# Kernel optimization log

Hardware: AMD Instinct MI355X
Metric: run time of the kernel (lower is better)

## Reference

```python
import jax, jax.numpy as jnp
import numpy as np

D_MODEL = 1024
N_HEADS = 16

def setup_inputs() -> dict:
    key = jax.random.key(0)
    ks = jax.random.split(key, 11)
    B, L, S, D = 2, 2048, 2048, D_MODEL
    s = 1.0 / np.sqrt(D)
    return {
        "Q": jax.random.normal(ks[0], (B, L, D), jnp.float32),
        "K": jax.random.normal(ks[1], (B, S, D), jnp.float32),
        "V": jax.random.normal(ks[2], (B, S, D), jnp.float32),
        "Wq": jax.random.normal(ks[3], (D, D), jnp.float32) * s,
        "bq": jnp.zeros((D,), jnp.float32),
        "Wk": jax.random.normal(ks[4], (D, D), jnp.float32) * s,
        "bk": jnp.zeros((D,), jnp.float32),
        "Wv": jax.random.normal(ks[5], (D, D), jnp.float32) * s,
        "bv": jnp.zeros((D,), jnp.float32),
        "We": jax.random.normal(ks[6], (D, D), jnp.float32) * s,
        "be": jnp.zeros((D,), jnp.float32),
    }

def reference(Q, K, V, Wq, bq, Wk, bk, Wv, bv, We, be):
    B, L, D = Q.shape
    S = K.shape[1]
    H = N_HEADS
    E = D // H
    # projections, split heads
    q = (Q @ Wq + bq).reshape(B, L, H, E)
    k = (K @ Wk + bk).reshape(B, S, H, E)
    v = (V @ Wv + bv).reshape(B, S, H, E)
    scale = 1.0 / np.sqrt(E)
    scores = jnp.einsum('blhe,bshe->bhls', q, k)  # [B,H,L,S]
    A = jax.nn.softmax(scale * scores, axis=-1)   # dropout is identity in eval
    out = jnp.einsum('bhls,bshd->blhd', A, v).reshape(B, L, H * E)
    return out @ We + be
```

## Files before the change

kernel.cpp:

```cpp
#include <hip/hip_runtime.h>
#include <hip/hip_bf16.h>
#include <stdint.h>

typedef __bf16 bf16_t;
typedef bf16_t bf16x8 __attribute__((ext_vector_type(8)));
typedef float  f32x4  __attribute__((ext_vector_type(4)));
typedef float  f32x16 __attribute__((ext_vector_type(16)));

#define GLOAD16(gp, lp) __builtin_amdgcn_global_load_lds( \
    (const __attribute__((address_space(1))) void*)(gp),  \
    (__attribute__((address_space(3))) void*)(lp), 16, 0, 0)

#define EXP2F(x) __builtin_amdgcn_exp2f(x)

__device__ inline uint32_t pack2(float lo, float hi) {
    union { bf16_t h[2]; uint32_t u; } x;
    x.h[0] = (bf16_t)lo; x.h[1] = (bf16_t)hi;
    return x.u;
}

__global__ __launch_bounds__(256) void wtrans_kernel(
    const float* __restrict__ Wq, const float* __restrict__ Wk,
    const float* __restrict__ Wv, const float* __restrict__ We,
    bf16_t* __restrict__ WqT, bf16_t* __restrict__ WkT,
    bf16_t* __restrict__ WvT, bf16_t* __restrict__ WeT)
{
    __shared__ bf16_t T[64][65];
    const float* W = (blockIdx.z == 0) ? Wq : (blockIdx.z == 1) ? Wk
                   : (blockIdx.z == 2) ? Wv : We;
    bf16_t* O = (blockIdx.z == 0) ? WqT : (blockIdx.z == 1) ? WkT
              : (blockIdx.z == 2) ? WvT : WeT;
    const int k0 = blockIdx.y * 64, n0 = blockIdx.x * 64;
    const int t = threadIdx.x;
    for (int i = 0; i < 16; ++i) {
        int flat = t + i * 256;
        int r = flat >> 6, c = flat & 63;
        T[r][c] = (bf16_t)W[(size_t)(k0 + r) * 1024 + n0 + c];
    }
    __syncthreads();
    for (int i = 0; i < 16; ++i) {
        int flat = t + i * 256;
        int n = flat >> 6, kk = flat & 63;
        O[(size_t)(n0 + n) * 1024 + k0 + kk] = T[kk][n];
    }
}

__global__ __launch_bounds__(256)
void cvt_kernel(const float* __restrict__ X0, const float* __restrict__ X1,
                const float* __restrict__ X2,
                bf16_t* __restrict__ Y0, bf16_t* __restrict__ Y1,
                bf16_t* __restrict__ Y2)
{
    const float* X = (blockIdx.y == 0) ? X0 : (blockIdx.y == 1) ? X1 : X2;
    bf16_t*      Y = (blockIdx.y == 0) ? Y0 : (blockIdx.y == 1) ? Y1 : Y2;
    size_t i0 = ((size_t)blockIdx.x * 256 + threadIdx.x) * 8;
    float4 v0 = *(const float4*)(X + i0);
    float4 v1 = *(const float4*)(X + i0 + 4);
    bf16x8 pv;
    pv[0] = (bf16_t)v0.x; pv[1] = (bf16_t)v0.y;
    pv[2] = (bf16_t)v0.z; pv[3] = (bf16_t)v0.w;
    pv[4] = (bf16_t)v1.x; pv[5] = (bf16_t)v1.y;
    pv[6] = (bf16_t)v1.z; pv[7] = (bf16_t)v1.w;
    *(bf16x8*)(Y + i0) = pv;
}

template<bool BATCHED>
__global__ __launch_bounds__(256)
void gemm3_kernel(const bf16_t* __restrict__ A0, const bf16_t* __restrict__ A1,
                  const bf16_t* __restrict__ A2,
                  const bf16_t* __restrict__ B0, const bf16_t* __restrict__ B1,
                  const bf16_t* __restrict__ B2,
                  const float* __restrict__ b0, const float* __restrict__ b1,
                  const float* __restrict__ b2,
                  void* __restrict__ C0, void* __restrict__ C1,
                  void* __restrict__ C2)
{
    constexpr int M = 4096, K = 1024, N = 1024;
    __shared__ bf16_t As[128 * 64];
    __shared__ bf16_t Bs[128 * 64];

    const int msel = BATCHED ? blockIdx.y : 0;
    const bf16_t* Ab   = (msel == 0) ? A0 : (msel == 1) ? A1 : A2;
    const bf16_t* Bt   = (msel == 0) ? B0 : (msel == 1) ? B1 : B2;
    const float*  bias = (msel == 0) ? b0 : (msel == 1) ? b1 : b2;
    void*         Cv   = (msel == 0) ? C0 : (msel == 1) ? C1 : C2;
    const int omode = BATCHED ? ((msel == 2) ? 2 : 0) : 1;

    const int xcd = blockIdx.x & 7, idx = blockIdx.x >> 3;
    const int bm = (xcd << 2) | (idx >> 3), bn = idx & 7;
    const int row0 = bm * 128, col0 = bn * 128;
    const int t = threadIdx.x, w = t >> 6, l = t & 63;
    const int wr = w >> 1, wc = w & 1;

    f32x4 acc[4][4];
    #pragma unroll
    for (int i = 0; i < 4; ++i)
        #pragma unroll
        for (int j = 0; j < 4; ++j)
            #pragma unroll
            for (int c = 0; c < 4; ++c) acc[i][j][c] = 0.f;

    for (int k0 = 0; k0 < K; k0 += 64) {
        #pragma unroll
        for (int i = 0; i < 4; ++i) {
            int chunk = (w * 4 + i) * 64 + l;
            int r = chunk >> 3, c = chunk & 7;
            int soff = (c ^ (r & 7)) * 8;
            GLOAD16(Ab + (size_t)(row0 + r) * K + k0 + soff, &As[(w * 4 + i) * 512]);
            GLOAD16(Bt + (size_t)(col0 + r) * K + k0 + soff, &Bs[(w * 4 + i) * 512]);
        }
        __syncthreads();

        #pragma unroll
        for (int eks = 0; eks < 2; ++eks) {
            bf16x8 af[4], bfv[4];
            #pragma unroll
            for (int mi = 0; mi < 4; ++mi) {
                int row = wr * 64 + mi * 16 + (l & 15);
                int sl = (eks * 4 + (l >> 4)) ^ (row & 7);
                af[mi] = *(const bf16x8*)&As[row * 64 + sl * 8];
            }
            #pragma unroll
            for (int ni = 0; ni < 4; ++ni) {
                int row = wc * 64 + ni * 16 + (l & 15);
                int sl = (eks * 4 + (l >> 4)) ^ (row & 7);
                bfv[ni] = *(const bf16x8*)&Bs[row * 64 + sl * 8];
            }
            __builtin_amdgcn_s_setprio(1);
            #pragma unroll
            for (int mi = 0; mi < 4; ++mi)
                #pragma unroll
                for (int ni = 0; ni < 4; ++ni)
                    acc[mi][ni] = __builtin_amdgcn_mfma_f32_16x16x32_bf16(
                        af[mi], bfv[ni], acc[mi][ni], 0, 0, 0);
            __builtin_amdgcn_s_setprio(0);
        }
        __syncthreads();
    }

    #pragma unroll
    for (int mi = 0; mi < 4; ++mi)
        #pragma unroll
        for (int ni = 0; ni < 4; ++ni) {
            int col = col0 + wc * 64 + ni * 16 + (l & 15);
            float bv = bias[col];
            int rowb = row0 + wr * 64 + mi * 16 + (l >> 4) * 4;
            if (omode == 2) {
                union { bf16_t h[4]; uint64_t q; } pk;
                #pragma unroll
                for (int j = 0; j < 4; ++j)
                    pk.h[j] = (bf16_t)(acc[mi][ni][j] + bv);
                *(uint64_t*)((bf16_t*)Cv + (size_t)col * M + rowb) = pk.q;
            } else if (omode == 1) {
                #pragma unroll
                for (int j = 0; j < 4; ++j)
                    ((float*)Cv)[(size_t)(rowb + j) * N + col] = acc[mi][ni][j] + bv;
            } else {
                #pragma unroll
                for (int j = 0; j < 4; ++j)
                    ((bf16_t*)Cv)[(size_t)(rowb + j) * N + col] = (bf16_t)(acc[mi][ni][j] + bv);
            }
        }
}

__global__ __launch_bounds__(256)
void attn7_kernel(const bf16_t* __restrict__ qp, const bf16_t* __restrict__ kp,
                  const bf16_t* __restrict__ vT, bf16_t* __restrict__ o)
{
    __shared__ bf16_t Ks[2][4096];
    __shared__ bf16_t Vs[2][4096];
    const int bid = blockIdx.x;
    const int xcd = bid & 7, j = bid >> 3;
    const int bh = (xcd << 2) | (j & 3);
    const int qb = j >> 2;
    const int b = bh >> 4, h = bh & 15;
    const int t = threadIdx.x, w = t >> 6, l = t & 63;
    const int ql = l & 31, hh = l >> 5;
    const float M0 = 8.0f * 1.44269504f;

    const bf16_t* kbase = kp + ((size_t)b * 2048) * 1024 + h * 64;
    const bf16_t* vbase = vT + ((size_t)h * 64) * 4096 + (size_t)b * 2048;
    const int q0 = qb * 128 + w * 32;

    bf16x8 qf[4];
    {
        const bf16_t* qrow = qp + ((size_t)b * 2048 + q0 + ql) * 1024 + h * 64;
        const float qs = 0.125f * 1.44269504f;
        #pragma unroll
        for (int eks = 0; eks < 4; ++eks) {
            bf16x8 v = *(const bf16x8*)(qrow + eks * 16 + hh * 8);
            #pragma unroll
            for (int jj = 0; jj < 8; ++jj) v[jj] = (bf16_t)((float)v[jj] * qs);
            qf[eks] = v;
        }
    }

    f32x16 acc0, acc1;
    #pragma unroll
    for (int r = 0; r < 16; ++r) { acc0[r] = 0.f; acc1[r] = 0.f; }
    float lsum = 0.f;

    const int ci0 = (w * 2) * 64 + l, ci1 = (w * 2 + 1) * 64 + l;
    const int gr0 = ci0 >> 3, gc0 = ci0 & 7, so0 = ((gc0 ^ (gr0 & 7)) * 8);
    const int gr1 = ci1 >> 3, gc1 = ci1 & 7, so1 = ((gc1 ^ (gr1 & 7)) * 8);

    GLOAD16(kbase + (size_t)gr0 * 1024 + so0, &Ks[0][(w * 2) * 512]);
    GLOAD16(kbase + (size_t)gr1 * 1024 + so1, &Ks[0][(w * 2 + 1) * 512]);
    GLOAD16(vbase + (size_t)gr0 * 4096 + so0, &Vs[0][(w * 2) * 512]);
    GLOAD16(vbase + (size_t)gr1 * 4096 + so1, &Vs[0][(w * 2 + 1) * 512]);
    __syncthreads();

    int cur = 0;
    for (int tile = 0; tile < 32; ++tile) {
        if (tile + 1 < 32) {
            const int s1 = (tile + 1) * 64;
            GLOAD16(kbase + (size_t)(s1 + gr0) * 1024 + so0, &Ks[cur ^ 1][(w * 2) * 512]);
            GLOAD16(kbase + (size_t)(s1 + gr1) * 1024 + so1, &Ks[cur ^ 1][(w * 2 + 1) * 512]);
            GLOAD16(vbase + (size_t)gr0 * 4096 + s1 + so0, &Vs[cur ^ 1][(w * 2) * 512]);
            GLOAD16(vbase + (size_t)gr1 * 4096 + s1 + so1, &Vs[cur ^ 1][(w * 2 + 1) * 512]);
        }

        f32x16 sA, sB;
        #pragma unroll
        for (int r = 0; r < 16; ++r) { sA[r] = -M0; sB[r] = -M0; }
        __builtin_amdgcn_s_setprio(1);
        #pragma unroll
        for (int eks = 0; eks < 4; ++eks) {
            bf16x8 k0 = *(const bf16x8*)&Ks[cur][ql * 64 + (((2 * eks + hh) ^ (ql & 7)) * 8)];
            bf16x8 k1 = *(const bf16x8*)&Ks[cur][(32 + ql) * 64 + (((2 * eks + hh) ^ (ql & 7)) * 8)];
            sA = __builtin_amdgcn_mfma_f32_32x32x16_bf16(k0, qf[eks], sA, 0, 0, 0);
            sB = __builtin_amdgcn_mfma_f32_32x32x16_bf16(k1, qf[eks], sB, 0, 0, 0);
        }
        __builtin_amdgcn_s_setprio(0);

        uint32_t wA[8], wB[8];
        float rs = 0.f;
        #pragma unroll
        for (int i = 0; i < 8; ++i) {
            float p0 = EXP2F(sA[2 * i]);
            float p1 = EXP2F(sA[2 * i + 1]);
            rs += p0 + p1;  wA[i] = pack2(p0, p1);
            float p2 = EXP2F(sB[2 * i]);
            float p3 = EXP2F(sB[2 * i + 1]);
            rs += p2 + p3;  wB[i] = pack2(p2, p3);
        }
        rs += __shfl_xor(rs, 32);
        lsum += rs;

        #pragma unroll
        for (int ks = 0; ks < 4; ++ks) {
            const int base = (ks & 1) * 4;
            uint32_t a0 = (ks < 2) ? wA[base]     : wB[base];
            uint32_t a1 = (ks < 2) ? wA[base + 1] : wB[base + 1];
            uint32_t a2 = (ks < 2) ? wA[base + 2] : wB[base + 2];
            uint32_t a3 = (ks < 2) ? wA[base + 3] : wB[base + 3];
            asm volatile("v_permlane32_swap_b32 %0, %1" : "+v"(a0), "+v"(a2));
            asm volatile("v_permlane32_swap_b32 %0, %1" : "+v"(a1), "+v"(a3));
            union { uint32_t u[4]; bf16x8 v; } pb;
            pb.u[0] = a0; pb.u[1] = a1; pb.u[2] = a2; pb.u[3] = a3;
            bf16x8 v0 = *(const bf16x8*)&Vs[cur][ql * 64 + (((2 * ks + hh) ^ (ql & 7)) * 8)];
            bf16x8 v1 = *(const bf16x8*)&Vs[cur][(32 + ql) * 64 + (((2 * ks + hh) ^ (ql & 7)) * 8)];
            __builtin_amdgcn_s_setprio(1);
            acc0 = __builtin_amdgcn_mfma_f32_32x32x16_bf16(v0, pb.v, acc0, 0, 0, 0);
            acc1 = __builtin_amdgcn_mfma_f32_32x32x16_bf16(v1, pb.v, acc1, 0, 0, 0);
            __builtin_amdgcn_s_setprio(0);
        }

        __syncthreads();
        cur ^= 1;
    }

    bf16_t* sc = &Ks[0][0];
    const float inv = 1.0f / lsum;
    #pragma unroll
    for (int r = 0; r < 16; ++r) {
        int e = (r & 3) + 8 * (r >> 2) + 4 * hh;
        sc[w * 2048 + ql * 64 + (((e >> 3) ^ (ql & 7)) * 8) + (e & 7)] =
            (bf16_t)(acc0[r] * inv);
        int e2 = e + 32;
        sc[w * 2048 + ql * 64 + (((e2 >> 3) ^ (ql & 7)) * 8) + (e2 & 7)] =
            (bf16_t)(acc1[r] * inv);
    }
    __syncthreads();
    #pragma unroll
    for (int it = 0; it < 4; ++it) {
        int ci = it * 64 + l;
        int qr = ci >> 3, ec = ci & 7;
        bf16x8 ov = *(const bf16x8*)&sc[w * 2048 + qr * 64 + ((ec ^ (qr & 7)) * 8)];
        *(bf16x8*)(o + ((size_t)b * 2048 + q0 + qr) * 1024 + h * 64 + ec * 8) = ov;
    }
}

extern "C" void kernel_launch(void* const* d_in, const int* in_sizes, int n_in,
                              void* d_out, int out_size, void* d_ws, size_t ws_size,
                              hipStream_t stream)
{
    const float* Q  = (const float*)d_in[0];
    const float* K  = (const float*)d_in[1];
    const float* V  = (const float*)d_in[2];
    const float* Wq = (const float*)d_in[3];
    const float* bq = (const float*)d_in[4];
    const float* Wk = (const float*)d_in[5];
    const float* bk = (const float*)d_in[6];
    const float* Wv = (const float*)d_in[7];
    const float* bv = (const float*)d_in[8];
    const float* We = (const float*)d_in[9];
    const float* be = (const float*)d_in[10];
    float* out = (float*)d_out;

    bf16_t* ws = (bf16_t*)d_ws;
    bf16_t* WqT = ws;
    bf16_t* WkT = WqT + 1024 * 1024;
    bf16_t* WvT = WkT + 1024 * 1024;
    bf16_t* WeT = WvT + 1024 * 1024;
    bf16_t* qp  = WeT + 1024 * 1024;
    bf16_t* kp  = qp  + 4096 * 1024;
    bf16_t* vt  = kp  + 4096 * 1024;
    bf16_t* ao  = vt  + 4096 * 1024;
    bf16_t* Qb  = ao  + 4096 * 1024;
    bf16_t* Kb  = Qb  + 4096 * 1024;
    bf16_t* Vb  = Kb  + 4096 * 1024;

    dim3 blk(256);

    hipLaunchKernelGGL(wtrans_kernel, dim3(16, 16, 4), blk, 0, stream,
                       Wq, Wk, Wv, We, WqT, WkT, WvT, WeT);

    hipLaunchKernelGGL(cvt_kernel, dim3(2048, 3), blk, 0, stream,
                       Q, K, V, Qb, Kb, Vb);

    hipLaunchKernelGGL((gemm3_kernel<true>), dim3(256, 3), blk, 0, stream,
                       Qb, Kb, Vb, WqT, WkT, WvT, bq, bk, bv,
                       (void*)qp, (void*)kp, (void*)vt);

    hipLaunchKernelGGL(attn7_kernel, dim3(512), blk, 0, stream,
                       qp, kp, vt, ao);

    hipLaunchKernelGGL((gemm3_kernel<false>), dim3(256, 1), blk, 0, stream,
                       ao, (const bf16_t*)nullptr, (const bf16_t*)nullptr,
                       WeT, (const bf16_t*)nullptr, (const bf16_t*)nullptr,
                       be, (const float*)nullptr, (const float*)nullptr,
                       (void*)out, (void*)nullptr, (void*)nullptr);
}
```

Before: 135.3 us.

## Compute softmax row sums via ones-MFMA and precompute LDS offsets

Replaces the per-tile VALU accumulation and cross-lane shuffle of softmax row sums with an extra MFMA that multiplies a vector of ones by the bf16 probability fragment, so the denominator comes out of the matrix unit. It also precomputes the swizzled LDS read offsets once and advances the global K/V prefetch pointers incrementally instead of recomputing addresses each tile. This trades VALU work for 50% more MFMA work in the PV stage. The denominator now sums the bf16-rounded probabilities, which matches what is multiplied with V.

```diff
diff --git a/kernel.cpp b/kernel.cpp
--- a/kernel.cpp
+++ b/kernel.cpp
@@ -164,7 +164,7 @@
 }
 
 __global__ __launch_bounds__(256)
-void attn7_kernel(const bf16_t* __restrict__ qp, const bf16_t* __restrict__ kp,
+void attn8_kernel(const bf16_t* __restrict__ qp, const bf16_t* __restrict__ kp,
                   const bf16_t* __restrict__ vT, bf16_t* __restrict__ o)
 {
     __shared__ bf16_t Ks[2][4096];
@@ -195,29 +195,45 @@
         }
     }
 
-    f32x16 acc0, acc1;
-    #pragma unroll
-    for (int r = 0; r < 16; ++r) { acc0[r] = 0.f; acc1[r] = 0.f; }
-    float lsum = 0.f;
+    bf16x8 onesv;
+    #pragma unroll
+    for (int jj = 0; jj < 8; ++jj) onesv[jj] = (bf16_t)1.0f;
+
+    f32x16 acc0, acc1, lacc;
+    #pragma unroll
+    for (int r = 0; r < 16; ++r) { acc0[r] = 0.f; acc1[r] = 0.f; lacc[r] = 0.f; }
+
+    int off_lo[4], off_hi[4];
+    #pragma unroll
+    for (int x = 0; x < 4; ++x) {
+        off_lo[x] = ql * 64 + (((2 * x + hh) ^ (ql & 7)) * 8);
+        off_hi[x] = (32 + ql) * 64 + (((2 * x + hh) ^ (ql & 7)) * 8);
+    }
 
     const int ci0 = (w * 2) * 64 + l, ci1 = (w * 2 + 1) * 64 + l;
     const int gr0 = ci0 >> 3, gc0 = ci0 & 7, so0 = ((gc0 ^ (gr0 & 7)) * 8);
     const int gr1 = ci1 >> 3, gc1 = ci1 & 7, so1 = ((gc1 ^ (gr1 & 7)) * 8);
 
-    GLOAD16(kbase + (size_t)gr0 * 1024 + so0, &Ks[0][(w * 2) * 512]);
-    GLOAD16(kbase + (size_t)gr1 * 1024 + so1, &Ks[0][(w * 2 + 1) * 512]);
-    GLOAD16(vbase + (size_t)gr0 * 4096 + so0, &Vs[0][(w * 2) * 512]);
-    GLOAD16(vbase + (size_t)gr1 * 4096 + so1, &Vs[0][(w * 2 + 1) * 512]);
+    const bf16_t* kq0 = kbase + (size_t)gr0 * 1024 + so0;
+    const bf16_t* kq1 = kbase + (size_t)gr1 * 1024 + so1;
+    const bf16_t* vq0 = vbase + (size_t)gr0 * 4096 + so0;
+    const bf16_t* vq1 = vbase + (size_t)gr1 * 4096 + so1;
+
+    GLOAD16(kq0, &Ks[0][(w * 2) * 512]);
+    GLOAD16(kq1, &Ks[0][(w * 2 + 1) * 512]);
+    GLOAD16(vq0, &Vs[0][(w * 2) * 512]);
+    GLOAD16(vq1, &Vs[0][(w * 2 + 1) * 512]);
     __syncthreads();
 
     int cur = 0;
     for (int tile = 0; tile < 32; ++tile) {
         if (tile + 1 < 32) {
-            const int s1 = (tile + 1) * 64;
-            GLOAD16(kbase + (size_t)(s1 + gr0) * 1024 + so0, &Ks[cur ^ 1][(w * 2) * 512]);
-            GLOAD16(kbase + (size_t)(s1 + gr1) * 1024 + so1, &Ks[cur ^ 1][(w * 2 + 1) * 512]);
-            GLOAD16(vbase + (size_t)gr0 * 4096 + s1 + so0, &Vs[cur ^ 1][(w * 2) * 512]);
-            GLOAD16(vbase + (size_t)gr1 * 4096 + s1 + so1, &Vs[cur ^ 1][(w * 2 + 1) * 512]);
+            kq0 += 64 * 1024; kq1 += 64 * 1024;
+            vq0 += 64;        vq1 += 64;
+            GLOAD16(kq0, &Ks[cur ^ 1][(w * 2) * 512]);
+            GLOAD16(kq1, &Ks[cur ^ 1][(w * 2 + 1) * 512]);
+            GLOAD16(vq0, &Vs[cur ^ 1][(w * 2) * 512]);
+            GLOAD16(vq1, &Vs[cur ^ 1][(w * 2 + 1) * 512]);
         }
 
         f32x16 sA, sB;
@@ -226,26 +242,19 @@
         __builtin_amdgcn_s_setprio(1);
         #pragma unroll
         for (int eks = 0; eks < 4; ++eks) {
-            bf16x8 k0 = *(const bf16x8*)&Ks[cur][ql * 64 + (((2 * eks + hh) ^ (ql & 7)) * 8)];
-            bf16x8 k1 = *(const bf16x8*)&Ks[cur][(32 + ql) * 64 + (((2 * eks + hh) ^ (ql & 7)) * 8)];
+            bf16x8 k0 = *(const bf16x8*)&Ks[cur][off_lo[eks]];
+            bf16x8 k1 = *(const bf16x8*)&Ks[cur][off_hi[eks]];
             sA = __builtin_amdgcn_mfma_f32_32x32x16_bf16(k0, qf[eks], sA, 0, 0, 0);
             sB = __builtin_amdgcn_mfma_f32_32x32x16_bf16(k1, qf[eks], sB, 0, 0, 0);
         }
         __builtin_amdgcn_s_setprio(0);
 
         uint32_t wA[8], wB[8];
-        float rs = 0.f;
         #pragma unroll
         for (int i = 0; i < 8; ++i) {
-            float p0 = EXP2F(sA[2 * i]);
-            float p1 = EXP2F(sA[2 * i + 1]);
-            rs += p0 + p1;  wA[i] = pack2(p0, p1);
-            float p2 = EXP2F(sB[2 * i]);
-            float p3 = EXP2F(sB[2 * i + 1]);
-            rs += p2 + p3;  wB[i] = pack2(p2, p3);
-        }
-        rs += __shfl_xor(rs, 32);
-        lsum += rs;
+            wA[i] = pack2(EXP2F(sA[2 * i]), EXP2F(sA[2 * i + 1]));
+            wB[i] = pack2(EXP2F(sB[2 * i]), EXP2F(sB[2 * i + 1]));
+        }
 
         #pragma unroll
         for (int ks = 0; ks < 4; ++ks) {
@@ -258,11 +267,12 @@
             asm volatile("v_permlane32_swap_b32 %0, %1" : "+v"(a1), "+v"(a3));
             union { uint32_t u[4]; bf16x8 v; } pb;
             pb.u[0] = a0; pb.u[1] = a1; pb.u[2] = a2; pb.u[3] = a3;
-            bf16x8 v0 = *(const bf16x8*)&Vs[cur][ql * 64 + (((2 * ks + hh) ^ (ql & 7)) * 8)];
-            bf16x8 v1 = *(const bf16x8*)&Vs[cur][(32 + ql) * 64 + (((2 * ks + hh) ^ (ql & 7)) * 8)];
+            bf16x8 v0 = *(const bf16x8*)&Vs[cur][off_lo[ks]];
+            bf16x8 v1 = *(const bf16x8*)&Vs[cur][off_hi[ks]];
             __builtin_amdgcn_s_setprio(1);
             acc0 = __builtin_amdgcn_mfma_f32_32x32x16_bf16(v0, pb.v, acc0, 0, 0, 0);
             acc1 = __builtin_amdgcn_mfma_f32_32x32x16_bf16(v1, pb.v, acc1, 0, 0, 0);
+            lacc = __builtin_amdgcn_mfma_f32_32x32x16_bf16(onesv, pb.v, lacc, 0, 0, 0);
             __builtin_amdgcn_s_setprio(0);
         }
 
@@ -271,7 +281,7 @@
     }
 
     bf16_t* sc = &Ks[0][0];
-    const float inv = 1.0f / lsum;
+    const float inv = 1.0f / lacc[0];
     #pragma unroll
     for (int r = 0; r < 16; ++r) {
         int e = (r & 3) + 8 * (r >> 2) + 4 * hh;
@@ -333,7 +343,7 @@
                        Qb, Kb, Vb, WqT, WkT, WvT, bq, bk, bv,
                        (void*)qp, (void*)kp, (void*)vt);
 
-    hipLaunchKernelGGL(attn7_kernel, dim3(512), blk, 0, stream,
+    hipLaunchKernelGGL(attn8_kernel, dim3(512), blk, 0, stream,
                        qp, kp, vt, ao);
 
     hipLaunchKernelGGL((gemm3_kernel<false>), dim3(256, 1), blk, 0, stream,
```

Result: no change. 134.5 us (-0.6%).
